# Optimization experiments

Hardware: AMD Instinct MI355X
Metric: run time of the kernel (lower is better)

The kernel has to match this reference:

```python
import jax, jax.numpy as jnp
import numpy as np

TAU, LBDA, THETA = 0.25, 0.15, 0.3
N_WARPS, N_ITERS = 5, 5
EPS = 1e-12  # GRAD_IS_ZERO


def centered_gradient(x):
    # centered [-0.5,0,0.5] stencil with one-sided boundaries (matches conv+boundary-fix)
    dx = jnp.concatenate([0.5 * (x[..., 1:2] - x[..., 0:1]),
                          0.5 * (x[..., 2:] - x[..., :-2]),
                          0.5 * (x[..., -1:] - x[..., -2:-1])], axis=-1)
    dy = jnp.concatenate([0.5 * (x[:, :, 1:2] - x[:, :, 0:1]),
                          0.5 * (x[:, :, 2:] - x[:, :, :-2]),
                          0.5 * (x[:, :, -1:] - x[:, :, -2:-1])], axis=2)
    return dx, dy


def forward_gradient(x):
    # [-1,1] forward difference, zero at last col/row (conv 'same' + zeroed last slice)
    dx = jnp.concatenate([x[..., 1:] - x[..., :-1], jnp.zeros_like(x[..., :1])], axis=-1)
    dy = jnp.concatenate([x[:, :, 1:] - x[:, :, :-1], jnp.zeros_like(x[:, :, :1])], axis=2)
    return dx, dy


def forward_divergence(px, py):
    # backward difference with zero left/top boundary; last entry = -p[-2]
    dx = jnp.concatenate([px[..., :1], px[..., 1:-1] - px[..., :-2], -px[..., -2:-1]], axis=-1)
    dy = jnp.concatenate([py[:, :, :1], py[:, :, 1:-1] - py[:, :, :-2], -py[:, :, -2:-1]], axis=2)
    return dx + dy


def warp_image(im, u, v):
    # bilinear warp by pixel flow (u,v); grid math mirrors the STN spatial_transformer:
    # normalized identity grid in [-1,1] plus flow*2/size, mapped back via (g+1)*size/2,
    # with indices clipped to the image (border behavior).
    B, C, H, W = im.shape
    dt = im.dtype
    gx = jnp.linspace(-1.0, 1.0, W, dtype=dt)[None, None, None, :]
    gy = jnp.linspace(-1.0, 1.0, H, dtype=dt)[None, None, :, None]
    x = (gx + u * (2.0 / W) + 1.0) * (W / 2.0)
    y = (gy + v * (2.0 / H) + 1.0) * (H / 2.0)
    x0 = jnp.floor(x).astype(jnp.int32)
    y0 = jnp.floor(y).astype(jnp.int32)
    x0i = jnp.clip(x0, 0, W - 1); x1i = jnp.clip(x0 + 1, 0, W - 1)
    y0i = jnp.clip(y0, 0, H - 1); y1i = jnp.clip(y0 + 1, 0, H - 1)
    x0f = x0i.astype(dt); x1f = x1i.astype(dt)
    y0f = y0i.astype(dt); y1f = y1i.astype(dt)
    flat = im.reshape(B, H * W)

    def gather(yi, xi):
        idx = (yi * W + xi).reshape(B, H * W)
        return jnp.take_along_axis(flat, idx, axis=1).reshape(B, C, H, W)

    Ia = gather(y0i, x0i); Ib = gather(y1i, x0i)
    Ic = gather(y0i, x1i); Id = gather(y1i, x1i)
    wa = (x1f - x) * (y1f - y); wb = (x1f - x) * (y - y0f)
    wc = (x - x0f) * (y1f - y); wd = (x - x0f) * (y - y0f)
    return wa * Ia + wb * Ib + wc * Ic + wd * Id


def tv_l1_scale(x1, x2, u1, u2):
    l_t = LBDA * THETA
    taut = TAU / THETA
    d2x, d2y = centered_gradient(x2)
    z = jnp.zeros_like(x1)
    p11, p12, p21, p22 = z, z, z, z
    rho = z
    for _ in range(N_WARPS):
        x2w = warp_image(x2, u1, u2)
        dxw = warp_image(d2x, u1, u2)
        dyw = warp_image(d2y, u1, u2)
        grad = dxw * dxw + dyw * dyw + EPS
        rho_c = x2w - dxw * u1 - dyw * u2 - x1
        for _ in range(N_ITERS):
            rho = rho_c + dxw * u1 + dyw * u2 + EPS
            m1 = rho < -l_t * grad
            m2 = rho > l_t * grad
            m3 = (~m1) & (~m2) & (grad > EPS)
            s = jnp.where(m1, l_t, jnp.where(m2, -l_t, jnp.where(m3, -rho / grad, 0.0)))
            v1 = s * dxw + u1
            v2 = s * dyw + u2
            u1 = v1 + THETA * forward_divergence(p11, p12)
            u2 = v2 + THETA * forward_divergence(p21, p22)
            u1x, u1y = forward_gradient(u1)
            u2x, u2y = forward_gradient(u2)
            n1 = 1.0 + taut * jnp.sqrt(u1x * u1x + u1y * u1y + EPS)
            n2 = 1.0 + taut * jnp.sqrt(u2x * u2x + u2y * u2y + EPS)
            p11 = (p11 + taut * u1x) / n1
            p12 = (p12 + taut * u1y) / n1
            p21 = (p21 + taut * u2x) / n2
            p22 = (p22 + taut * u2y) / n2
    return u1, u2, rho


def setup_inputs() -> dict:
    key = jax.random.key(0)
    k1, k2 = jax.random.split(key)
    B, H, W = 8, 480, 480
    x1 = jax.random.uniform(k1, (B, 1, H, W), dtype=jnp.float32)
    x2 = jax.random.uniform(k2, (B, 1, H, W), dtype=jnp.float32)
    u1 = jnp.zeros((B, 1, H, W), dtype=jnp.float32)
    u2 = jnp.zeros((B, 1, H, W), dtype=jnp.float32)
    return {"x1": x1, "x2": x2, "u1": u1, "u2": u2}


def reference(x1, x2, u1, u2):
    return tv_l1_scale(x1, x2, u1, u2)
```

## Files before the change

kernel.cpp:

```cpp
#include <hip/hip_runtime.h>

#pragma clang fp contract(off)


constexpr int B = 8, H = 480, W = 480;
constexpr int HW = H * W;
constexpr int N = B * HW;

constexpr float THETA = (float)0.3;
constexpr float L_T  = (float)(0.15 * 0.3);
constexpr float TAUT = (float)(0.25 / 0.3);
constexpr float EPSF = (float)1e-12;

#define RW 50
#define RH 40
#define HALO 5
#define TW 40
#define TH 30
#define NTX 12
#define NTY 16
#define TPB 512
#define NPX 4
#define RPX (RW*RH)

template <int WARPK, bool INTERIOR>
__device__ __forceinline__ void run_body(
    const float* __restrict__ x1, const float* __restrict__ x2,
    const float* __restrict__ u1In, const float* __restrict__ u2In,
    const float2* __restrict__ uIn, const float4* __restrict__ pIn,
    float* __restrict__ u1Out, float* __restrict__ u2Out,
    float2* __restrict__ uOut, float4* __restrict__ pOut,
    float* __restrict__ rhoOut,
    int bx, int by, int b,
    float2* __restrict__ su, float2* __restrict__ spA,
    float2* __restrict__ spB)
{
  const int ox = bx * TW - HALO;
  const int oy = by * TH - HALO;
  const int tid = threadIdx.x;
  const int base = b * HW;
  const float* __restrict__ im = x2 + base;

  float cdx[NPX], cdy[NPX], crc[NPX];
  int lxA[NPX], lyA[NPX];
#pragma unroll
  for (int k = 0; k < NPX; ++k) {
    int idx = tid + k * TPB;
    lyA[k] = idx / RW;
    lxA[k] = idx - lyA[k] * RW;
  }

#pragma unroll
  for (int k = 0; k < NPX; ++k) {
    int idx = tid + k * TPB;
    if (idx < RPX) {
      int lx = lxA[k], ly = lyA[k];
      int px = ox + lx, py = oy + ly;
      bool valid = INTERIOR ? true : (px >= 0 && px < W && py >= 0 && py < H);
      if (valid) {
        int gi = base + py * W + px;
        float u, v;
        if (WARPK == 0) { u = u1In[gi]; v = u2In[gi]; }
        else            { float2 uv = uIn[gi]; u = uv.x; v = uv.y; }
        const float step = 2.0f / 479.0f;
        float gx = -1.0f + (float)px * step;
        float gy = -1.0f + (float)py * step;
        float X = ((gx + u * (float)(2.0 / 480.0)) + 1.0f) * 240.0f;
        float Y = ((gy + v * (float)(2.0 / 480.0)) + 1.0f) * 240.0f;
        float fX = floorf(X), fY = floorf(Y);
        int ix = (int)fX, iy = (int)fY;
        int x0i = min(max(ix, 0), W - 1);
        int x1i = min(max(ix + 1, 0), W - 1);
        int y0i = min(max(iy, 0), H - 1);
        int y1i = min(max(iy + 1, 0), H - 1);
        float x0f = (float)x0i, x1f = (float)x1i;
        float y0f = (float)y0i, y1f = (float)y1i;
        float wa = (x1f - X) * (y1f - Y);
        float wb = (x1f - X) * (Y - y0f);
        float wc = (X - x0f) * (y1f - Y);
        float wd = (X - x0f) * (Y - y0f);
        auto at = [&](int yy, int xx) -> float { return im[yy * W + xx]; };
        auto dxc = [&](int yy, int xx) -> float {
          int xm = max(xx - 1, 0), xp = min(xx + 1, W - 1);
          return 0.5f * (at(yy, xp) - at(yy, xm));
        };
        auto dyc = [&](int yy, int xx) -> float {
          int ym = max(yy - 1, 0), yp = min(yy + 1, H - 1);
          return 0.5f * (at(yp, xx) - at(ym, xx));
        };
        float x2w = ((wa * at(y0i, x0i) + wb * at(y1i, x0i)) + wc * at(y0i, x1i)) + wd * at(y1i, x1i);
        float dxw = ((wa * dxc(y0i, x0i) + wb * dxc(y1i, x0i)) + wc * dxc(y0i, x1i)) + wd * dxc(y1i, x1i);
        float dyw = ((wa * dyc(y0i, x0i) + wb * dyc(y1i, x0i)) + wc * dyc(y0i, x1i)) + wd * dyc(y1i, x1i);
        cdx[k] = dxw; cdy[k] = dyw;
        crc[k] = ((x2w - dxw * u) - dyw * v) - x1[gi];
        float4 q;
        if (WARPK == 0) q = make_float4(0.f, 0.f, 0.f, 0.f);
        else            q = pIn[gi];
        su[idx]  = make_float2(u, v);
        spA[idx] = make_float2(q.x, q.z);
        spB[idx] = make_float2(q.y, q.w);
      }
    }
  }
  __syncthreads();

  for (int t = 1; t <= 5; ++t) {
    int ulox, uloy, uhix, uhiy;
    if (INTERIOR) {
      ulox = ox + t; uloy = oy + t;
      uhix = ox + RW + 1 - t; uhiy = oy + RH + 1 - t;
    } else {
      ulox = ox + t; if (ulox < 0) ulox = 0;
      uloy = oy + t; if (uloy < 0) uloy = 0;
      uhix = (ox + RW >= W) ? W : (ox + RW + 1 - t);
      uhiy = (oy + RH >= H) ? H : (oy + RH + 1 - t);
    }

#pragma unroll
    for (int k = 0; k < NPX; ++k) {
      int idx = tid + k * TPB;
      if (idx < RPX) {
        int lx = lxA[k], ly = lyA[k];
        int px = ox + lx, py = oy + ly;
        if (px >= ulox && px < uhix && py >= uloy && py < uhiy) {
          float2 uo  = su[idx];
          float2 pAo = spA[idx];
          float2 pBo = spB[idx];
          float2 pl = spA[idx - 1];
          float2 pu = spB[idx - RW];
          float dx = cdx[k], dy = cdy[k];
          float u = uo.x, v = uo.y;
          float rho = ((crc[k] + dx * u) + dy * v) + EPSF;
          float grad = (dx * dx + dy * dy) + EPSF;
          float lt_g = L_T * grad;
          float s;
          if (rho < -lt_g)      s = L_T;
          else if (rho > lt_g)  s = -L_T;
          else if (grad > EPSF) s = (-rho) / grad;
          else                  s = 0.f;
          float v1 = s * dx + u;
          float v2 = s * dy + v;
          float dvx1, dvy1, dvx2, dvy2;
          if (INTERIOR) {
            dvx1 = pAo.x - pl.x;
            dvy1 = pBo.x - pu.x;
            dvx2 = pAo.y - pl.y;
            dvy2 = pBo.y - pu.y;
          } else {
            if (px == 0)          dvx1 = pAo.x;
            else if (px == W - 1) dvx1 = -pl.x;
            else                  dvx1 = pAo.x - pl.x;
            if (py == 0)          dvy1 = pBo.x;
            else if (py == H - 1) dvy1 = -pu.x;
            else                  dvy1 = pBo.x - pu.x;
            if (px == 0)          dvx2 = pAo.y;
            else if (px == W - 1) dvx2 = -pl.y;
            else                  dvx2 = pAo.y - pl.y;
            if (py == 0)          dvy2 = pBo.y;
            else if (py == H - 1) dvy2 = -pu.y;
            else                  dvy2 = pBo.y - pu.y;
          }
          float nu1 = v1 + THETA * (dvx1 + dvy1);
          float nu2 = v2 + THETA * (dvx2 + dvy2);
          su[idx] = make_float2(nu1, nu2);
          if (WARPK == 2 && t == 5) {
            if (lx >= HALO && lx < HALO + TW && ly >= HALO && ly < HALO + TH)
              rhoOut[base + py * W + px] = rho;
          }
        }
      }
    }
    __syncthreads();

    if (!(WARPK == 2 && t == 5)) {
      int phix, phiy;
      if (INTERIOR) { phix = ox + RW - t; phiy = oy + RH - t; }
      else {
        phix = (ox + RW >= W) ? W : (ox + RW - t);
        phiy = (oy + RH >= H) ? H : (oy + RH - t);
      }
#pragma unroll
      for (int k = 0; k < NPX; ++k) {
        int idx = tid + k * TPB;
        if (idx < RPX) {
          int lx = lxA[k], ly = lyA[k];
          int px = ox + lx, py = oy + ly;
          if (px >= ulox && px < phix && py >= uloy && py < phiy) {
            float2 uo = su[idx];
            float2 uR = su[idx + 1];
            float2 uD = su[idx + RW];
            float2 pAo = spA[idx];
            float2 pBo = spB[idx];
            float u1c = uo.x, u2c = uo.y;
            float u1x, u1y, u2x, u2y;
            if (INTERIOR) {
              u1x = uR.x - u1c; u1y = uD.x - u1c;
              u2x = uR.y - u2c; u2y = uD.y - u2c;
            } else {
              u1x = (px < W - 1) ? uR.x - u1c : 0.f;
              u1y = (py < H - 1) ? uD.x - u1c : 0.f;
              u2x = (px < W - 1) ? uR.y - u2c : 0.f;
              u2y = (py < H - 1) ? uD.y - u2c : 0.f;
            }
            float n1 = 1.0f + TAUT * sqrtf((u1x * u1x + u1y * u1y) + EPSF);
            float n2 = 1.0f + TAUT * sqrtf((u2x * u2x + u2y * u2y) + EPSF);
            float np11 = (pAo.x + TAUT * u1x) / n1;
            float np12 = (pBo.x + TAUT * u1y) / n1;
            float np21 = (pAo.y + TAUT * u2x) / n2;
            float np22 = (pBo.y + TAUT * u2y) / n2;
            spA[idx] = make_float2(np11, np21);
            spB[idx] = make_float2(np12, np22);
          }
        }
      }
    }
    __syncthreads();
  }

#pragma unroll
  for (int k = 0; k < NPX; ++k) {
    int idx = tid + k * TPB;
    if (idx < RPX) {
      int lx = lxA[k], ly = lyA[k];
      if (lx >= HALO && lx < HALO + TW && ly >= HALO && ly < HALO + TH) {
        int gi = base + (oy + ly) * W + (ox + lx);
        float2 uo = su[idx];
        if (WARPK == 2) {
          u1Out[gi] = uo.x;
          u2Out[gi] = uo.y;
        } else {
          uOut[gi] = uo;
          float2 a = spA[idx], c = spB[idx];
          pOut[gi] = make_float4(a.x, c.x, a.y, c.y);
        }
      }
    }
  }
}

template <int WARPK>
__global__ __launch_bounds__(TPB, 4) void k_fused(
    const float* __restrict__ x1, const float* __restrict__ x2,
    const float* __restrict__ u1In, const float* __restrict__ u2In,
    const float2* __restrict__ uIn, const float4* __restrict__ pIn,
    float* __restrict__ u1Out, float* __restrict__ u2Out,
    float2* __restrict__ uOut, float4* __restrict__ pOut,
    float* __restrict__ rhoOut)
{
  __shared__ float2 su[RPX], spA[RPX], spB[RPX];
  int blk = blockIdx.x;
  int bx = blk % NTX;
  int by = (blk / NTX) % NTY;
  int b  = blk / (NTX * NTY);
  bool interior = (bx > 0 && bx < NTX - 1 && by > 0 && by < NTY - 1);
  if (interior)
    run_body<WARPK, true >(x1, x2, u1In, u2In, uIn, pIn, u1Out, u2Out,
                           uOut, pOut, rhoOut, bx, by, b, su, spA, spB);
  else
    run_body<WARPK, false>(x1, x2, u1In, u2In, uIn, pIn, u1Out, u2Out,
                           uOut, pOut, rhoOut, bx, by, b, su, spA, spB);
}

extern "C" void kernel_launch(void* const* d_in, const int* in_sizes, int n_in,
                              void* d_out, int out_size, void* d_ws, size_t ws_size,
                              hipStream_t stream) {
  const float* x1 = (const float*)d_in[0];
  const float* x2 = (const float*)d_in[1];
  const float* u1_in = (const float*)d_in[2];
  const float* u2_in = (const float*)d_in[3];

  float* u1o  = (float*)d_out;
  float* u2o  = u1o + (size_t)N;
  float* rhoo = u1o + (size_t)2 * N;

  float* ws  = (float*)d_ws;
  float2* uA = (float2*)ws;
  float4* pA = (float4*)(ws + (size_t)2 * N);
  float2* uB = (float2*)(ws + (size_t)6 * N);
  float4* pB = (float4*)(ws + (size_t)8 * N);

  dim3 grd(NTX * NTY * B), blk(TPB);
  k_fused<0><<<grd, blk, 0, stream>>>(x1, x2, u1_in, u2_in, nullptr, nullptr,
                                      nullptr, nullptr, uA, pA, rhoo);
  k_fused<1><<<grd, blk, 0, stream>>>(x1, x2, nullptr, nullptr, uA, pA,
                                      nullptr, nullptr, uB, pB, rhoo);
  k_fused<1><<<grd, blk, 0, stream>>>(x1, x2, nullptr, nullptr, uB, pB,
                                      nullptr, nullptr, uA, pA, rhoo);
  k_fused<1><<<grd, blk, 0, stream>>>(x1, x2, nullptr, nullptr, uA, pA,
                                      nullptr, nullptr, uB, pB, rhoo);
  k_fused<2><<<grd, blk, 0, stream>>>(x1, x2, nullptr, nullptr, uB, pB,
                                      u1o, u2o, nullptr, nullptr, rhoo);
}
```

Measured before the change: 365.9 us.

## Shrink tile width and drop interior/boundary template split

Tile width drops from 40 to 32 (region 42x40), so each block holds fewer pixels in shared memory and the grid grows to 15 tiles across. The separate INTERIOR/boundary template instantiations are merged into one kernel that always runs the boundary checks. Per-thread stored tile coordinates are recomputed on the fly, and the warp gather loads are flattened into explicit index math. The aim is to cut register use and shared memory for better occupancy, at the cost of a larger share of redundant halo work and extra branches in interior tiles.

```diff
diff --git a/kernel.cpp b/kernel.cpp
--- a/kernel.cpp
+++ b/kernel.cpp
@@ -12,29 +12,34 @@
 constexpr float TAUT = (float)(0.25 / 0.3);
 constexpr float EPSF = (float)1e-12;
 
-#define RW 50
+#define RW 42
 #define RH 40
 #define HALO 5
-#define TW 40
+#define TW 32
 #define TH 30
-#define NTX 12
+#define NTX 15
 #define NTY 16
 #define TPB 512
 #define NPX 4
 #define RPX (RW*RH)
 
-template <int WARPK, bool INTERIOR>
-__device__ __forceinline__ void run_body(
+template <int WARPK>
+__global__ __launch_bounds__(TPB, 4) void k_fused(
     const float* __restrict__ x1, const float* __restrict__ x2,
     const float* __restrict__ u1In, const float* __restrict__ u2In,
     const float2* __restrict__ uIn, const float4* __restrict__ pIn,
     float* __restrict__ u1Out, float* __restrict__ u2Out,
     float2* __restrict__ uOut, float4* __restrict__ pOut,
-    float* __restrict__ rhoOut,
-    int bx, int by, int b,
-    float2* __restrict__ su, float2* __restrict__ spA,
-    float2* __restrict__ spB)
+    float* __restrict__ rhoOut)
 {
+  __shared__ float2 su[RPX];
+  __shared__ float2 spA[RPX];
+  __shared__ float2 spB[RPX];
+
+  int blk = blockIdx.x;
+  int bx = blk % NTX;
+  int by = (blk / NTX) % NTY;
+  int b  = blk / (NTX * NTY);
   const int ox = bx * TW - HALO;
   const int oy = by * TH - HALO;
   const int tid = threadIdx.x;
@@ -42,21 +47,14 @@
   const float* __restrict__ im = x2 + base;
 
   float cdx[NPX], cdy[NPX], crc[NPX];
-  int lxA[NPX], lyA[NPX];
-#pragma unroll
-  for (int k = 0; k < NPX; ++k) {
-    int idx = tid + k * TPB;
-    lyA[k] = idx / RW;
-    lxA[k] = idx - lyA[k] * RW;
-  }
 
 #pragma unroll
   for (int k = 0; k < NPX; ++k) {
     int idx = tid + k * TPB;
     if (idx < RPX) {
-      int lx = lxA[k], ly = lyA[k];
+      int ly = idx / RW, lx = idx - ly * RW;
       int px = ox + lx, py = oy + ly;
-      bool valid = INTERIOR ? true : (px >= 0 && px < W && py >= 0 && py < H);
+      bool valid = (px >= 0 && px < W && py >= 0 && py < H);
       if (valid) {
         int gi = base + py * W + px;
         float u, v;
@@ -79,18 +77,25 @@
         float wb = (x1f - X) * (Y - y0f);
         float wc = (X - x0f) * (y1f - Y);
         float wd = (X - x0f) * (Y - y0f);
-        auto at = [&](int yy, int xx) -> float { return im[yy * W + xx]; };
-        auto dxc = [&](int yy, int xx) -> float {
-          int xm = max(xx - 1, 0), xp = min(xx + 1, W - 1);
-          return 0.5f * (at(yy, xp) - at(yy, xm));
-        };
-        auto dyc = [&](int yy, int xx) -> float {
-          int ym = max(yy - 1, 0), yp = min(yy + 1, H - 1);
-          return 0.5f * (at(yp, xx) - at(ym, xx));
-        };
-        float x2w = ((wa * at(y0i, x0i) + wb * at(y1i, x0i)) + wc * at(y0i, x1i)) + wd * at(y1i, x1i);
-        float dxw = ((wa * dxc(y0i, x0i) + wb * dxc(y1i, x0i)) + wc * dxc(y0i, x1i)) + wd * dxc(y1i, x1i);
-        float dyw = ((wa * dyc(y0i, x0i) + wb * dyc(y1i, x0i)) + wc * dyc(y0i, x1i)) + wd * dyc(y1i, x1i);
+        int xmA = max(x0i - 1, 0), xpA = min(x0i + 1, W - 1);
+        int xmB = max(x1i - 1, 0), xpB = min(x1i + 1, W - 1);
+        int ymA = max(y0i - 1, 0), ypA = min(y0i + 1, H - 1);
+        int ymB = max(y1i - 1, 0), ypB = min(y1i + 1, H - 1);
+        int y0W = y0i * W, y1W = y1i * W;
+        int ymAW = ymA * W, ypAW = ypA * W, ymBW = ymB * W, ypBW = ypB * W;
+        float Ia = im[y0W + x0i], Ib = im[y1W + x0i];
+        float Ic = im[y0W + x1i], Id = im[y1W + x1i];
+        float dA = 0.5f * (im[y0W + xpA] - im[y0W + xmA]);
+        float dB = 0.5f * (im[y1W + xpA] - im[y1W + xmA]);
+        float dC = 0.5f * (im[y0W + xpB] - im[y0W + xmB]);
+        float dD = 0.5f * (im[y1W + xpB] - im[y1W + xmB]);
+        float eA = 0.5f * (im[ypAW + x0i] - im[ymAW + x0i]);
+        float eB = 0.5f * (im[ypBW + x0i] - im[ymBW + x0i]);
+        float eC = 0.5f * (im[ypAW + x1i] - im[ymAW + x1i]);
+        float eD = 0.5f * (im[ypBW + x1i] - im[ymBW + x1i]);
+        float x2w = ((wa * Ia + wb * Ib) + wc * Ic) + wd * Id;
+        float dxw = ((wa * dA + wb * dB) + wc * dC) + wd * dD;
+        float dyw = ((wa * eA + wb * eB) + wc * eC) + wd * eD;
         cdx[k] = dxw; cdy[k] = dyw;
         crc[k] = ((x2w - dxw * u) - dyw * v) - x1[gi];
         float4 q;
@@ -105,22 +110,16 @@
   __syncthreads();
 
   for (int t = 1; t <= 5; ++t) {
-    int ulox, uloy, uhix, uhiy;
-    if (INTERIOR) {
-      ulox = ox + t; uloy = oy + t;
-      uhix = ox + RW + 1 - t; uhiy = oy + RH + 1 - t;
-    } else {
-      ulox = ox + t; if (ulox < 0) ulox = 0;
-      uloy = oy + t; if (uloy < 0) uloy = 0;
-      uhix = (ox + RW >= W) ? W : (ox + RW + 1 - t);
-      uhiy = (oy + RH >= H) ? H : (oy + RH + 1 - t);
-    }
+    int ulox = ox + t; if (ulox < 0) ulox = 0;
+    int uloy = oy + t; if (uloy < 0) uloy = 0;
+    int uhix = (ox + RW >= W) ? W : (ox + RW + 1 - t);
+    int uhiy = (oy + RH >= H) ? H : (oy + RH + 1 - t);
 
 #pragma unroll
     for (int k = 0; k < NPX; ++k) {
       int idx = tid + k * TPB;
       if (idx < RPX) {
-        int lx = lxA[k], ly = lyA[k];
+        int ly = idx / RW, lx = idx - ly * RW;
         int px = ox + lx, py = oy + ly;
         if (px >= ulox && px < uhix && py >= uloy && py < uhiy) {
           float2 uo  = su[idx];
@@ -141,25 +140,18 @@
           float v1 = s * dx + u;
           float v2 = s * dy + v;
           float dvx1, dvy1, dvx2, dvy2;
-          if (INTERIOR) {
-            dvx1 = pAo.x - pl.x;
-            dvy1 = pBo.x - pu.x;
-            dvx2 = pAo.y - pl.y;
-            dvy2 = pBo.y - pu.y;
-          } else {
-            if (px == 0)          dvx1 = pAo.x;
-            else if (px == W - 1) dvx1 = -pl.x;
-            else                  dvx1 = pAo.x - pl.x;
-            if (py == 0)          dvy1 = pBo.x;
-            else if (py == H - 1) dvy1 = -pu.x;
-            else                  dvy1 = pBo.x - pu.x;
-            if (px == 0)          dvx2 = pAo.y;
-            else if (px == W - 1) dvx2 = -pl.y;
-            else                  dvx2 = pAo.y - pl.y;
-            if (py == 0)          dvy2 = pBo.y;
-            else if (py == H - 1) dvy2 = -pu.y;
-            else                  dvy2 = pBo.y - pu.y;
-          }
+          if (px == 0)          dvx1 = pAo.x;
+          else if (px == W - 1) dvx1 = -pl.x;
+          else                  dvx1 = pAo.x - pl.x;
+          if (py == 0)          dvy1 = pBo.x;
+          else if (py == H - 1) dvy1 = -pu.x;
+          else                  dvy1 = pBo.x - pu.x;
+          if (px == 0)          dvx2 = pAo.y;
+          else if (px == W - 1) dvx2 = -pl.y;
+          else                  dvx2 = pAo.y - pl.y;
+          if (py == 0)          dvy2 = pBo.y;
+          else if (py == H - 1) dvy2 = -pu.y;
+          else                  dvy2 = pBo.y - pu.y;
           float nu1 = v1 + THETA * (dvx1 + dvy1);
           float nu2 = v2 + THETA * (dvx2 + dvy2);
           su[idx] = make_float2(nu1, nu2);
@@ -173,17 +165,13 @@
     __syncthreads();
 
     if (!(WARPK == 2 && t == 5)) {
-      int phix, phiy;
-      if (INTERIOR) { phix = ox + RW - t; phiy = oy + RH - t; }
-      else {
-        phix = (ox + RW >= W) ? W : (ox + RW - t);
-        phiy = (oy + RH >= H) ? H : (oy + RH - t);
-      }
+      int phix = (ox + RW >= W) ? W : (ox + RW - t);
+      int phiy = (oy + RH >= H) ? H : (oy + RH - t);
 #pragma unroll
       for (int k = 0; k < NPX; ++k) {
         int idx = tid + k * TPB;
         if (idx < RPX) {
-          int lx = lxA[k], ly = lyA[k];
+          int ly = idx / RW, lx = idx - ly * RW;
           int px = ox + lx, py = oy + ly;
           if (px >= ulox && px < phix && py >= uloy && py < phiy) {
             float2 uo = su[idx];
@@ -192,16 +180,10 @@
             float2 pAo = spA[idx];
             float2 pBo = spB[idx];
             float u1c = uo.x, u2c = uo.y;
-            float u1x, u1y, u2x, u2y;
-            if (INTERIOR) {
-              u1x = uR.x - u1c; u1y = uD.x - u1c;
-              u2x = uR.y - u2c; u2y = uD.y - u2c;
-            } else {
-              u1x = (px < W - 1) ? uR.x - u1c : 0.f;
-              u1y = (py < H - 1) ? uD.x - u1c : 0.f;
-              u2x = (px < W - 1) ? uR.y - u2c : 0.f;
-              u2y = (py < H - 1) ? uD.y - u2c : 0.f;
-            }
+            float u1x = (px < W - 1) ? uR.x - u1c : 0.f;
+            float u1y = (py < H - 1) ? uD.x - u1c : 0.f;
+            float u2x = (px < W - 1) ? uR.y - u2c : 0.f;
+            float u2y = (py < H - 1) ? uD.y - u2c : 0.f;
             float n1 = 1.0f + TAUT * sqrtf((u1x * u1x + u1y * u1y) + EPSF);
             float n2 = 1.0f + TAUT * sqrtf((u2x * u2x + u2y * u2y) + EPSF);
             float np11 = (pAo.x + TAUT * u1x) / n1;
@@ -221,7 +203,7 @@
   for (int k = 0; k < NPX; ++k) {
     int idx = tid + k * TPB;
     if (idx < RPX) {
-      int lx = lxA[k], ly = lyA[k];
+      int ly = idx / RW, lx = idx - ly * RW;
       if (lx >= HALO && lx < HALO + TW && ly >= HALO && ly < HALO + TH) {
         int gi = base + (oy + ly) * W + (ox + lx);
         float2 uo = su[idx];
@@ -236,29 +218,6 @@
       }
     }
   }
-}
-
-template <int WARPK>
-__global__ __launch_bounds__(TPB, 4) void k_fused(
-    const float* __restrict__ x1, const float* __restrict__ x2,
-    const float* __restrict__ u1In, const float* __restrict__ u2In,
-    const float2* __restrict__ uIn, const float4* __restrict__ pIn,
-    float* __restrict__ u1Out, float* __restrict__ u2Out,
-    float2* __restrict__ uOut, float4* __restrict__ pOut,
-    float* __restrict__ rhoOut)
-{
-  __shared__ float2 su[RPX], spA[RPX], spB[RPX];
-  int blk = blockIdx.x;
-  int bx = blk % NTX;
-  int by = (blk / NTX) % NTY;
-  int b  = blk / (NTX * NTY);
-  bool interior = (bx > 0 && bx < NTX - 1 && by > 0 && by < NTY - 1);
-  if (interior)
-    run_body<WARPK, true >(x1, x2, u1In, u2In, uIn, pIn, u1Out, u2Out,
-                           uOut, pOut, rhoOut, bx, by, b, su, spA, spB);
-  else
-    run_body<WARPK, false>(x1, x2, u1In, u2In, uIn, pIn, u1Out, u2Out,
-                           uOut, pOut, rhoOut, bx, by, b, su, spA, spB);
 }
 
 extern "C" void kernel_launch(void* const* d_in, const int* in_sizes, int n_in,
```

Measured after the change: 367.4 us. Within noise of the previous version (+0.4%).
